# Kernel optimization log

Measured on AMD Instinct MI355X. Metric: run time of the kernel, lower is better.

The kernel has to match this reference:

```python
import jax, jax.numpy as jnp
import numpy as np

D_MODEL = 768; D_STATE = 64; D_CONV = 7; EXPAND = 2; HEADDIM = 64; NGROUPS = 1; CHUNK = 256
D_INNER = EXPAND * D_MODEL                                      # 1536
NHEADS = D_INNER // HEADDIM                                     # 24
D_IN_PROJ = 2 * D_INNER + 2 * NGROUPS * D_STATE + 2 * NHEADS    # 3248
CONV_DIM = D_INNER + 2 * NGROUPS * D_STATE                      # 1664
BATCH, SEQLEN = 2, 4096
EPS = 1e-5


def setup_inputs() -> dict:
    key = jax.random.key(0)
    ks = jax.random.split(key, 8)
    w = lambda k, shape, s=0.02: jax.random.normal(k, shape, jnp.float32) * s
    # dt in [1e-3, 1e-1], dt_bias = softplus^{-1}(dt)
    dt0 = jnp.exp(jax.random.uniform(ks[3], (NHEADS,)) * (np.log(0.1) - np.log(0.001)) + np.log(0.001))
    return {
        "x": jax.random.normal(ks[0], (BATCH, SEQLEN, D_MODEL), jnp.float32),
        "ln_w": jnp.ones((D_MODEL,), jnp.float32),
        "ln_b": jnp.zeros((D_MODEL,), jnp.float32),
        "in_proj_w": w(ks[1], (D_IN_PROJ, D_MODEL)),
        "conv_w": w(ks[2], (CONV_DIM, D_CONV), 0.2),
        "conv_b": jnp.zeros((CONV_DIM,), jnp.float32),
        "dt_bias": dt0 + jnp.log(-jnp.expm1(-dt0)),
        "A_log": jnp.log(jax.random.uniform(ks[4], (NHEADS,), minval=1.0, maxval=16.0)),
        "D": jnp.ones((NHEADS,), jnp.float32),
        "fc_D_w": w(ks[5], (NHEADS, D_INNER)),
        "rms_w": jnp.ones((D_INNER,), jnp.float32),
        "out_proj_w": w(ks[6], (D_MODEL, D_INNER)),
    }


def _segsum(a):
    # a: (..., T) -> (..., T, T) lower-triangular segment sums, -inf above diagonal
    T = a.shape[-1]
    cs = jnp.cumsum(a, -1)
    ss = cs[..., :, None] - cs[..., None, :]
    return jnp.where(jnp.tril(jnp.ones((T, T), bool)), ss, -jnp.inf)


def _ssd(X, A, Bm, Cm):
    # Chunked SSD scan (mamba_chunk_scan_combined, D=None, z=None, ngroups=1).
    # X: (b,l,h,p) already scaled by dt; A: (b,l,h) = dt*A_head; Bm,Cm: (b,l,n)
    b, l, h, p = X.shape
    c = l // CHUNK
    X = X.reshape(b, c, CHUNK, h, p)
    A = A.reshape(b, c, CHUNK, h).transpose(0, 3, 1, 2)  # (b,h,c,l)
    Bm = Bm.reshape(b, c, CHUNK, D_STATE)
    Cm = Cm.reshape(b, c, CHUNK, D_STATE)
    A_cum = jnp.cumsum(A, -1)
    Lmat = jnp.exp(_segsum(A))                                      # (b,h,c,l,s)
    Y_diag = jnp.einsum("bcln,bcsn,bhcls,bcshp->bclhp", Cm, Bm, Lmat, X)
    decay_states = jnp.exp(A_cum[..., -1:] - A_cum)                 # (b,h,c,l)
    states = jnp.einsum("bcln,bhcl,bclhp->bchpn", Bm, decay_states, X)
    A_chunk = jnp.pad(A_cum[..., -1], ((0, 0), (0, 0), (1, 0)))     # (b,h,c+1)
    decay_chunk = jnp.exp(_segsum(A_chunk))                         # (b,h,c+1,c+1)
    all_states = jnp.concatenate([jnp.zeros_like(states[:, :1]), states], 1)
    prev = jnp.einsum("bhzc,bchpn->bzhpn", decay_chunk, all_states)[:, :-1]
    Y_off = jnp.einsum("bcln,bchpn,bhcl->bclhp", Cm, prev, jnp.exp(A_cum))
    return (Y_diag + Y_off).reshape(b, l, h, p)


def _dwconv_causal(x, w, b):
    # x: (B,L,C), w: (C,K); torch Conv1d(padding=K-1) then [:, :L] == causal conv
    xp = jnp.pad(x, ((0, 0), (D_CONV - 1, 0), (0, 0))).transpose(0, 2, 1)
    y = jax.lax.conv_general_dilated(xp, w[:, None, :], (1,), "VALID",
                                     feature_group_count=CONV_DIM,
                                     dimension_numbers=("NCH", "OIH", "NCH"))
    return y.transpose(0, 2, 1) + b


def _forward(x, ln_w, ln_b, in_proj_w, conv_w, conv_b, dt_bias, A_log, D, fc_D_w, rms_w, out_proj_w):
    B, L, _ = x.shape
    # pre-LayerNorm
    mu = jnp.mean(x, -1, keepdims=True)
    var = jnp.mean((x - mu) ** 2, -1, keepdims=True)
    u = (x - mu) * jax.lax.rsqrt(var + EPS) * ln_w + ln_b
    # input projection -> z | xBC | dt_fw,dt_bw
    zxbcdt = u @ in_proj_w.T
    z = zxbcdt[..., :D_INNER]
    xBC = zxbcdt[..., D_INNER:D_INNER + CONV_DIM]
    dt2 = zxbcdt[..., -2 * NHEADS:]
    dt = jnp.concatenate([dt2[..., :NHEADS], jnp.flip(dt2[..., NHEADS:], 1)], 0)  # (2B,L,H)
    dt = jax.nn.softplus(dt + dt_bias)
    A = -jnp.exp(A_log)
    # causal depthwise conv + SiLU
    xBC = jax.nn.silu(_dwconv_causal(xBC, conv_w, conv_b))
    xs = xBC[..., :D_INNER]
    Bm = xBC[..., D_INNER:D_INNER + D_STATE]
    Cm = xBC[..., D_INNER + D_STATE:]
    x_og = xs
    cat2 = lambda t: jnp.concatenate([t, jnp.flip(t, 1)], 0)  # fwd + reversed copy
    X = cat2(xs).reshape(2 * B, L, NHEADS, HEADDIM) * dt[..., None]
    y = _ssd(X, dt * A, cat2(Bm), cat2(Cm)).reshape(2 * B, L, D_INNER)
    # quasiseparable combine: shift each direction by one, zero the boundary
    y = jnp.roll(y, 1, axis=1).at[:, 0, :].set(0.0)
    y = y[:B] + jnp.flip(y[B:], 1)
    # data-dependent diagonal term
    Dterm = x_og @ fc_D_w.T + D                                 # (B,L,H)
    y = y + x_og * jnp.repeat(Dterm, HEADDIM, axis=-1)
    # gated RMSNorm
    y = y * jax.nn.silu(z)
    y = y * jax.lax.rsqrt(jnp.mean(y * y, -1, keepdims=True) + EPS) * rms_w
    # out projection + residual (dropout=0 -> identity)
    return y @ out_proj_w.T + x


def reference(x, ln_w, ln_b, in_proj_w, conv_w, conv_b, dt_bias, A_log, D, fc_D_w, rms_w, out_proj_w):
    return _forward(x, ln_w, ln_b, in_proj_w, conv_w, conv_b, dt_bias, A_log, D, fc_D_w, rms_w, out_proj_w)
```

## Files before the change

kernel.cpp:

```cpp
#include <hip/hip_runtime.h>
#include <hip/hip_bf16.h>
#include <cstdint>
#include <cstddef>

typedef __hip_bfloat16 bf16;
typedef __attribute__((ext_vector_type(8))) short short8;
typedef __attribute__((ext_vector_type(4))) float f32x4;

#define B_   2
#define L_   4096
#define DM_  768
#define DI_  1536
#define NH_  24
#define HD_  64
#define DS_  64
#define CH_  256
#define NC_  16
#define CD_  1664
#define DIP_ 3248
#define EPS_ 1e-5f

#define ROWS_ (B_*L_)
#define BB4_  (2*B_)

#define LDSK 40
#define LDT  72

__device__ __forceinline__ float b2f(bf16 v) { return __bfloat162float(v); }
__device__ __forceinline__ bf16  f2b(float v) { return __float2bfloat16(v); }
__device__ __forceinline__ float sb2f(short s) {
    bf16 t; __builtin_memcpy(&t, &s, 2); return __bfloat162float(t);
}
__device__ __forceinline__ short f2s(float v) {
    bf16 t = __float2bfloat16(v); short s; __builtin_memcpy(&s, &t, 2); return s;
}

__global__ __launch_bounds__(256) void cast_f2b(const float* __restrict__ s,
                                                bf16* __restrict__ d, int n) {
    int i = (blockIdx.x * 256 + threadIdx.x) * 4;
    if (i + 3 < n) {
        float4 v = *(const float4*)(s + i);
        d[i]   = f2b(v.x); d[i+1] = f2b(v.y);
        d[i+2] = f2b(v.z); d[i+3] = f2b(v.w);
    } else {
        for (int k = i; k < n; k++) d[k] = f2b(s[k]);
    }
}

__global__ __launch_bounds__(256) void ln_kernel(const float* __restrict__ x,
                                                 const float* __restrict__ w,
                                                 const float* __restrict__ bb,
                                                 bf16* __restrict__ u) {
    int row = blockIdx.x, tid = threadIdx.x;
    const float* xr = x + (size_t)row * DM_;
    float v0 = xr[tid], v1 = xr[tid + 256], v2 = xr[tid + 512];
    float s = v0 + v1 + v2;
    float q = v0*v0 + v1*v1 + v2*v2;
    for (int off = 32; off > 0; off >>= 1) {
        s += __shfl_down(s, off);
        q += __shfl_down(q, off);
    }
    __shared__ float rs[4], rq[4];
    __shared__ float mean_s, rstd_s;
    int lane = tid & 63, wid = tid >> 6;
    if (!lane) { rs[wid] = s; rq[wid] = q; }
    __syncthreads();
    if (!tid) {
        float S = rs[0]+rs[1]+rs[2]+rs[3];
        float Q = rq[0]+rq[1]+rq[2]+rq[3];
        float mu = S / (float)DM_;
        float var = Q / (float)DM_ - mu*mu;
        mean_s = mu; rstd_s = rsqrtf(var + EPS_);
    }
    __syncthreads();
    float mu = mean_s, rstd = rstd_s;
    bf16* ur = u + (size_t)row * DM_;
    ur[tid]       = f2b((v0 - mu) * rstd * w[tid]       + bb[tid]);
    ur[tid + 256] = f2b((v1 - mu) * rstd * w[tid + 256] + bb[tid + 256]);
    ur[tid + 512] = f2b((v2 - mu) * rstd * w[tid + 512] + bb[tid + 512]);
}

__global__ __launch_bounds__(256) void gemm_bf16_inproj(const bf16* __restrict__ A,
                                                        const bf16* __restrict__ W,
                                                        bf16* __restrict__ zbuf,
                                                        bf16* __restrict__ xbc,
                                                        float* __restrict__ dtr) {
    __shared__ short As[128 * LDSK];
    __shared__ short Ws[128 * LDSK];
    int tid = threadIdx.x;
    int wave = tid >> 6, lane = tid & 63;
    int wm = (wave >> 1) * 64, wn = (wave & 1) * 64;
    int bm = blockIdx.y * 128, bn = blockIdx.x * 128;
    f32x4 acc[4][4] = {};
    int lr = tid >> 1;
    int lseg = (tid & 1) * 16;
    const int K = DM_;
    int fr = lane & 15, kg = (lane >> 4) * 8;
    for (int k0 = 0; k0 < K; k0 += 32) {
        const short* ag = (const short*)A + (size_t)(bm + lr) * K + k0 + lseg;
        short8 av0 = *(const short8*)ag;
        short8 av1 = *(const short8*)(ag + 8);
        short8 wv0 = {}, wv1 = {};
        int n = bn + lr;
        if (n < DIP_) {
            const short* wg = (const short*)W + (size_t)n * K + k0 + lseg;
            wv0 = *(const short8*)wg;
            wv1 = *(const short8*)(wg + 8);
        }
        __syncthreads();
        *(short8*)&As[lr*LDSK + lseg]     = av0;
        *(short8*)&As[lr*LDSK + lseg + 8] = av1;
        *(short8*)&Ws[lr*LDSK + lseg]     = wv0;
        *(short8*)&Ws[lr*LDSK + lseg + 8] = wv1;
        __syncthreads();
        short8 af[4], wf[4];
        #pragma unroll
        for (int i = 0; i < 4; i++)
            af[i] = *(const short8*)&As[(wm + i*16 + fr)*LDSK + kg];
        #pragma unroll
        for (int j = 0; j < 4; j++)
            wf[j] = *(const short8*)&Ws[(wn + j*16 + fr)*LDSK + kg];
        #pragma unroll
        for (int i = 0; i < 4; i++)
            #pragma unroll
            for (int j = 0; j < 4; j++)
                acc[i][j] = __builtin_amdgcn_mfma_f32_16x16x32_bf16(af[i], wf[j], acc[i][j], 0, 0, 0);
    }
    int rg = (lane >> 4) * 4;
    #pragma unroll
    for (int i = 0; i < 4; i++) {
        int mrow = bm + wm + i*16 + rg;
        #pragma unroll
        for (int j = 0; j < 4; j++) {
            int ncol = bn + wn + j*16 + fr;
            #pragma unroll
            for (int r = 0; r < 4; r++) {
                float v = acc[i][j][r];
                int m = mrow + r;
                if (ncol < DI_)            zbuf[(size_t)m * DI_ + ncol] = f2b(v);
                else if (ncol < DI_ + CD_) xbc[(size_t)m * CD_ + (ncol - DI_)] = f2b(v);
                else if (ncol < DIP_)      dtr[(size_t)m * 48 + (ncol - DI_ - CD_)] = v;
            }
        }
    }
}

__global__ __launch_bounds__(256) void gemm_bf16_out(const bf16* __restrict__ A,
                                                     const bf16* __restrict__ W,
                                                     const float* __restrict__ resid,
                                                     float* __restrict__ C) {
    __shared__ short As[128 * LDSK];
    __shared__ short Ws[128 * LDSK];
    int tid = threadIdx.x;
    int wave = tid >> 6, lane = tid & 63;
    int wm = (wave >> 1) * 64, wn = (wave & 1) * 64;
    int bm = blockIdx.y * 128, bn = blockIdx.x * 128;
    f32x4 acc[4][4] = {};
    int lr = tid >> 1;
    int lseg = (tid & 1) * 16;
    const int K = DI_;
    int fr = lane & 15, kg = (lane >> 4) * 8;
    for (int k0 = 0; k0 < K; k0 += 32) {
        const short* ag = (const short*)A + (size_t)(bm + lr) * K + k0 + lseg;
        short8 av0 = *(const short8*)ag;
        short8 av1 = *(const short8*)(ag + 8);
        const short* wg = (const short*)W + (size_t)(bn + lr) * K + k0 + lseg;
        short8 wv0 = *(const short8*)wg;
        short8 wv1 = *(const short8*)(wg + 8);
        __syncthreads();
        *(short8*)&As[lr*LDSK + lseg]     = av0;
        *(short8*)&As[lr*LDSK + lseg + 8] = av1;
        *(short8*)&Ws[lr*LDSK + lseg]     = wv0;
        *(short8*)&Ws[lr*LDSK + lseg + 8] = wv1;
        __syncthreads();
        short8 af[4], wf[4];
        #pragma unroll
        for (int i = 0; i < 4; i++)
            af[i] = *(const short8*)&As[(wm + i*16 + fr)*LDSK + kg];
        #pragma unroll
        for (int j = 0; j < 4; j++)
            wf[j] = *(const short8*)&Ws[(wn + j*16 + fr)*LDSK + kg];
        #pragma unroll
        for (int i = 0; i < 4; i++)
            #pragma unroll
            for (int j = 0; j < 4; j++)
                acc[i][j] = __builtin_amdgcn_mfma_f32_16x16x32_bf16(af[i], wf[j], acc[i][j], 0, 0, 0);
    }
    int rg = (lane >> 4) * 4;
    #pragma unroll
    for (int i = 0; i < 4; i++) {
        int mrow = bm + wm + i*16 + rg;
        #pragma unroll
        for (int j = 0; j < 4; j++) {
            int ncol = bn + wn + j*16 + fr;
            #pragma unroll
            for (int r = 0; r < 4; r++) {
                int m = mrow + r;
                C[(size_t)m * DM_ + ncol] = acc[i][j][r] + resid[(size_t)m * DM_ + ncol];
            }
        }
    }
}

__global__ __launch_bounds__(256) void conv_kernel(const bf16* __restrict__ xbc,
                                                   const float* __restrict__ cw,
                                                   const float* __restrict__ cb,
                                                   bf16* __restrict__ out) {
    int g = blockIdx.x * 256 + threadIdx.x;
    int cg = g % 208;
    int tq = g / 208;
    int b = tq >> 10;
    int t0 = (tq & 1023) * 4;
    int c8 = cg * 8;
    const short* src = (const short*)xbc + (size_t)(b * L_) * CD_ + c8;

    float w[7][8], acc[4][8];
    #pragma unroll
    for (int k = 0; k < 8; k++) {
        #pragma unroll
        for (int j = 0; j < 7; j++) w[j][k] = cw[(c8 + k) * 7 + j];
        float bias = cb[c8 + k];
        #pragma unroll
        for (int q = 0; q < 4; q++) acc[q][k] = bias;
    }
    #pragma unroll
    for (int m = 0; m < 10; m++) {
        int tt = t0 - 6 + m;
        float row[8];
        if (tt >= 0) {
            short8 v = *(const short8*)(src + (size_t)tt * CD_);
            #pragma unroll
            for (int k = 0; k < 8; k++) row[k] = sb2f(v[k]);
        } else {
            #pragma unroll
            for (int k = 0; k < 8; k++) row[k] = 0.f;
        }
        #pragma unroll
        for (int q = 0; q < 4; q++) {
            int j = m - q;
            if (j >= 0 && j < 7) {
                #pragma unroll
                for (int k = 0; k < 8; k++) acc[q][k] += row[k] * w[j][k];
            }
        }
    }
    #pragma unroll
    for (int q = 0; q < 4; q++) {
        short8 o;
        #pragma unroll
        for (int k = 0; k < 8; k++) {
            float a = acc[q][k];
            a = a / (1.f + __expf(-a));
            o[k] = f2s(a);
        }
        *(short8*)((short*)out + (size_t)(b * L_ + t0 + q) * CD_ + c8) = o;
    }
}

__global__ __launch_bounds__(256) void dt_kernel(const float* __restrict__ dtr,
                                                 const float* __restrict__ dt_bias,
                                                 float* __restrict__ dt4) {
    int idx = blockIdx.x * 256 + threadIdx.x;
    if (idx >= BB4_ * L_ * NH_) return;
    int h = idx % NH_;
    int t = (idx / NH_) % L_;
    int bbx = idx / (NH_ * L_);
    int bp = bbx & 1;
    float raw;
    if (bbx < 2) raw = dtr[((size_t)(bp * L_ + t)) * 48 + h];
    else         raw = dtr[((size_t)(bp * L_ + (L_ - 1 - t))) * 48 + NH_ + h];
    float v = raw + dt_bias[h];
    float dt = (v > 20.f) ? v : log1pf(__expf(v));
    dt4[idx] = dt;
}

__global__ __launch_bounds__(256) void scan_kernel(const float* __restrict__ dt4,
                                                   const float* __restrict__ A_log,
                                                   float* __restrict__ Acum) {
    int bid = blockIdx.x;
    int c  = bid % NC_;
    int h  = (bid / NC_) % NH_;
    int bbx = bid / (NC_ * NH_);
    int l = threadIdx.x;
    float Ah = -__expf(A_log[h]);
    float val = dt4[((size_t)(bbx * L_) + c * CH_ + l) * NH_ + h] * Ah;
    __shared__ float sc[256];
    sc[l] = val; __syncthreads();
    for (int off = 1; off < 256; off <<= 1) {
        float t = (l >= off) ? sc[l - off] : 0.f;
        __syncthreads();
        sc[l] += t;
        __syncthreads();
    }
    Acum[(size_t)bid * CH_ + l] = sc[l];
}

__global__ __launch_bounds__(256) void xt_kernel(const bf16* __restrict__ conv,
                                                 const float* __restrict__ dt4,
                                                 bf16* __restrict__ XT,
                                                 bf16* __restrict__ BT) {
    int bid = blockIdx.x;
    int hh = bid % 25;
    int c  = (bid / 25) % NC_;
    int bbx = bid / (25 * NC_);
    int bp = bbx & 1;
    bool flip = bbx >= 2;
    bool isB = (hh == NH_);
    int coff = isB ? DI_ : hh * HD_;
    int tid = threadIdx.x;
    __shared__ short tile[64][72];
    short* dstb = (short*)(isB ? BT : XT);
    size_t rowbase = isB ? (size_t)(bbx * 64) : (size_t)((bbx * NH_ + hh) * 64);
    for (int lt = 0; lt < 4; lt++) {
        __syncthreads();
        #pragma unroll
        for (int it = 0; it < 2; it++) {
            int li = tid + it * 256;
            int r = li >> 3, seg = (li & 7) * 8;
            int t = c * CH_ + lt * 64 + r;
            int tt = flip ? (L_ - 1 - t) : t;
            short8 v = *(const short8*)((const short*)conv + (size_t)(bp * L_ + tt) * CD_ + coff + seg);
            if (!isB) {
                float dtv = dt4[((size_t)(bbx * L_) + t) * NH_ + hh];
                #pragma unroll
                for (int k = 0; k < 8; k++) v[k] = f2s(sb2f(v[k]) * dtv);
            }
            *(short8*)&tile[r][seg] = v;
        }
        __syncthreads();
        #pragma unroll
        for (int it = 0; it < 2; it++) {
            int li = tid + it * 256;
            int p = li >> 3, seg = (li & 7) * 8;
            short8 o;
            #pragma unroll
            for (int k = 0; k < 8; k++) o[k] = tile[seg + k][p];
            *(short8*)(dstb + (rowbase + p) * L_ + c * CH_ + lt * 64 + seg) = o;
        }
    }
}

__global__ __launch_bounds__(256) void states_kernel(const bf16* __restrict__ XT,
                                                     const bf16* __restrict__ BT,
                                                     const float* __restrict__ Acum,
                                                     bf16* __restrict__ states) {
    int bid = blockIdx.x;
    int h = bid % NH_;
    int c = (bid / NH_) % NC_;
    int bbx = bid / (NH_ * NC_);
    int tid = threadIdx.x;
    int wave = tid >> 6, lane = tid & 63;
    int wr = wave >> 1, wc = wave & 1;
    int fr = lane & 15, kg = (lane >> 4) * 8, rg = (lane >> 4) * 4;
    size_t abase = ((size_t)(bbx * NH_ + h) * NC_ + c) * CH_;
    __shared__ float dec[256];
    {
        float Atot = Acum[abase + CH_ - 1];
        dec[tid] = __expf(Atot - Acum[abase + tid]);
    }
    __syncthreads();
    const short* xbase = (const short*)XT + (size_t)((bbx * NH_ + h) * 64) * L_ + c * CH_;
    const short* bbase = (const short*)BT + (size_t)(bbx * 64) * L_ + c * CH_;
    f32x4 acc[2][2] = {};
    for (int lt = 0; lt < 4; lt++) {
        #pragma unroll
        for (int ks = 0; ks < 2; ks++) {
            int l0 = lt * 64 + ks * 32 + kg;
            float d[8];
            #pragma unroll
            for (int k = 0; k < 8; k++) d[k] = dec[l0 + k];
            short8 af[2], wf[2];
            #pragma unroll
            for (int i = 0; i < 2; i++)
                af[i] = *(const short8*)(xbase + (size_t)(wr*32 + i*16 + fr) * L_ + l0);
            #pragma unroll
            for (int j = 0; j < 2; j++) {
                short8 raw = *(const short8*)(bbase + (size_t)(wc*32 + j*16 + fr) * L_ + l0);
                #pragma unroll
                for (int k = 0; k < 8; k++) raw[k] = f2s(sb2f(raw[k]) * d[k]);
                wf[j] = raw;
            }
            #pragma unroll
            for (int i = 0; i < 2; i++)
                #pragma unroll
                for (int j = 0; j < 2; j++)
                    acc[i][j] = __builtin_amdgcn_mfma_f32_16x16x32_bf16(af[i], wf[j], acc[i][j], 0, 0, 0);
        }
    }
    size_t sbase = (size_t)bid * 4096;
    #pragma unroll
    for (int i = 0; i < 2; i++)
        #pragma unroll
        for (int j = 0; j < 2; j++)
            #pragma unroll
            for (int r = 0; r < 4; r++) {
                int p = wr*32 + i*16 + rg + r;
                int n = wc*32 + j*16 + fr;
                states[sbase + p*64 + n] = f2b(acc[i][j][r]);
            }
}

__global__ __launch_bounds__(256) void chunkscan_kernel(bf16* __restrict__ sp,
                                                        const float* __restrict__ Acum) {
    int bid = blockIdx.x;
    int h = bid % NH_;
    int bbx = bid / NH_;
    int tid = threadIdx.x;
    float run[16];
    #pragma unroll
    for (int k = 0; k < 16; k++) run[k] = 0.f;
    for (int c = 0; c < NC_; c++) {
        float Tc = Acum[((size_t)(bbx * NH_ + h) * NC_ + c) * CH_ + CH_ - 1];
        float ec = __expf(Tc);
        size_t base = ((size_t)(bbx * NC_ + c) * NH_ + h) * 4096;
        #pragma unroll
        for (int k = 0; k < 16; k++) {
            size_t e = tid + k * 256;
            float sv = b2f(sp[base + e]);
            sp[base + e] = f2b(run[k]);
            run[k] = run[k] * ec + sv;
        }
    }
}

__global__ __launch_bounds__(256) void ydiag_kernel(const bf16* __restrict__ conv,
                                                    const bf16* __restrict__ XT,
                                                    const float* __restrict__ Acum,
                                                    const bf16* __restrict__ prev,
                                                    bf16* __restrict__ yc,
                                                    int pass) {
    int bid = blockIdx.x;
    int lt = bid & 3;
    int q  = bid >> 2;
    int h  = q % NH_;
    int r2 = q / NH_;
    int c  = r2 % NC_;
    int b  = r2 / NC_;
    int bbx = pass ? (b + 2) : b;
    int bp = b;
    bool flip = pass != 0;
    int tid = threadIdx.x;
    int wave = tid >> 6, lane = tid & 63;
    int wr = wave >> 1, wc = wave & 1;
    int fr = lane & 15, kg = (lane >> 4) * 8, rg = (lane >> 4) * 4;
    size_t abase = ((size_t)(bbx * NH_ + h) * NC_ + c) * CH_;

    __shared__ short Gt[64 * LDT];
    __shared__ float aL[64], aS[64];
    if (tid < 64) aL[tid] = Acum[abase + lt * 64 + tid];

    short8 cf[2][2];
    #pragma unroll
    for (int i = 0; i < 2; i++) {
        int l = wr*32 + i*16 + fr;
        int t = c * CH_ + lt * 64 + l;
        int tt = flip ? (L_ - 1 - t) : t;
        const short* crow = (const short*)conv + (size_t)(bp * L_ + tt) * CD_ + DI_ + DS_;
        #pragma unroll
        for (int ks = 0; ks < 2; ks++)
            cf[i][ks] = *(const short8*)(crow + ks*32 + kg);
    }

    f32x4 acc[2][2] = {};
    size_t pbase = ((size_t)(bbx * NC_ + c) * NH_ + h) * 4096;
    #pragma unroll
    for (int ks = 0; ks < 2; ks++) {
        #pragma unroll
        for (int j = 0; j < 2; j++) {
            short8 pf = *(const short8*)((const short*)prev + pbase + (size_t)(wc*32 + j*16 + fr)*64 + ks*32 + kg);
            #pragma unroll
            for (int i = 0; i < 2; i++)
                acc[i][j] = __builtin_amdgcn_mfma_f32_16x16x32_bf16(cf[i][ks], pf, acc[i][j], 0, 0, 0);
        }
    }
    __syncthreads();
    #pragma unroll
    for (int i = 0; i < 2; i++)
        #pragma unroll
        for (int r = 0; r < 4; r++) {
            float e = __expf(aL[wr*32 + i*16 + rg + r]);
            #pragma unroll
            for (int j = 0; j < 2; j++) acc[i][j][r] *= e;
        }

    const short* xbase = (const short*)XT + (size_t)((bbx * NH_ + h) * 64) * L_ + c * CH_;

    for (int st = 0; st <= lt; st++) {
        if (tid < 64) aS[tid] = Acum[abase + st * 64 + tid];
        f32x4 gacc[2][2] = {};
        #pragma unroll
        for (int j = 0; j < 2; j++) {
            int s = wc*32 + j*16 + fr;
            int t = c * CH_ + st * 64 + s;
            int tt = flip ? (L_ - 1 - t) : t;
            const short* brow = (const short*)conv + (size_t)(bp * L_ + tt) * CD_ + DI_;
            #pragma unroll
            for (int ks = 0; ks < 2; ks++) {
                short8 bf = *(const short8*)(brow + ks*32 + kg);
                #pragma unroll
                for (int i = 0; i < 2; i++)
                    gacc[i][j] = __builtin_amdgcn_mfma_f32_16x16x32_bf16(cf[i][ks], bf, gacc[i][j], 0, 0, 0);
            }
        }
        __syncthreads();
        #pragma unroll
        for (int i = 0; i < 2; i++)
            #pragma unroll
            for (int j = 0; j < 2; j++)
                #pragma unroll
                for (int r = 0; r < 4; r++) {
                    int ll = wr*32 + i*16 + rg + r;
                    int ss = wc*32 + j*16 + fr;
                    bool valid = (st < lt) || (ll >= ss);
                    float g = valid ? gacc[i][j][r] * __expf(aL[ll] - aS[ss]) : 0.f;
                    Gt[ll * LDT + ss] = f2s(g);
                }
        __syncthreads();
        #pragma unroll
        for (int ks = 0; ks < 2; ks++) {
            short8 gf[2], xf[2];
            #pragma unroll
            for (int i = 0; i < 2; i++)
                gf[i] = *(const short8*)&Gt[(wr*32 + i*16 + fr)*LDT + ks*32 + kg];
            #pragma unroll
            for (int j = 0; j < 2; j++)
                xf[j] = *(const short8*)(xbase + (size_t)(wc*32 + j*16 + fr)*L_ + st*64 + ks*32 + kg);
            #pragma unroll
            for (int i = 0; i < 2; i++)
                #pragma unroll
                for (int j = 0; j < 2; j++)
                    acc[i][j] = __builtin_amdgcn_mfma_f32_16x16x32_bf16(gf[i], xf[j], acc[i][j], 0, 0, 0);
        }
        __syncthreads();
    }

    #pragma unroll
    for (int i = 0; i < 2; i++)
        #pragma unroll
        for (int r = 0; r < 4; r++) {
            int l = wr*32 + i*16 + rg + r;
            int t = c * CH_ + lt * 64 + l;
            #pragma unroll
            for (int j = 0; j < 2; j++) {
                int p = wc*32 + j*16 + fr;
                float v = acc[i][j][r];
                if (!pass) {
                    int pos = t + 1;
                    if (pos == L_)
                        yc[((size_t)(b * L_)) * DI_ + h * HD_ + p] = f2b(0.f);
                    else
                        yc[((size_t)(b * L_) + pos) * DI_ + h * HD_ + p] = f2b(v);
                } else {
                    int pos = L_ - 2 - t;
                    if (pos >= 0) {
                        size_t o = ((size_t)(b * L_) + pos) * DI_ + h * HD_ + p;
                        yc[o] = f2b(b2f(yc[o]) + v);
                    }
                }
            }
        }
}

__global__ __launch_bounds__(256) void combine_kernel(const bf16* __restrict__ yc,
                                                      const bf16* __restrict__ conv,
                                                      const bf16* __restrict__ zbuf,
                                                      const float* __restrict__ fcD,
                                                      const float* __restrict__ Dvec,
                                                      const float* __restrict__ rms_w,
                                                      bf16* __restrict__ ybuf) {
    int row = blockIdx.x;
    int tid = threadIdx.x;
    __shared__ float xog_s[DI_];
    __shared__ float dterm_s[NH_];
    __shared__ float rs[4];
    __shared__ float scale_s;
    float yv[6], xog[6], zv[6];
    const bf16* convrow = conv + (size_t)row * CD_;
    const bf16* zrow = zbuf + (size_t)row * DI_;
    const bf16* ycrow = yc + (size_t)row * DI_;
    #pragma unroll
    for (int k = 0; k < 6; k++) {
        int d = tid + k * 256;
        float xo = b2f(convrow[d]);
        xog[k] = xo; xog_s[d] = xo;
        zv[k] = b2f(zrow[d]);
        yv[k] = b2f(ycrow[d]);
    }
    __syncthreads();
    int wid = tid >> 6, lane = tid & 63;
    for (int hh = 0; hh < 6; hh++) {
        int h = wid * 6 + hh;
        float s = 0.f;
        #pragma unroll
        for (int k = 0; k < 24; k++) {
            int d = lane + k * 64;
            s += xog_s[d] * fcD[(size_t)h * DI_ + d];
        }
        for (int off = 32; off > 0; off >>= 1) s += __shfl_down(s, off);
        if (!lane) dterm_s[h] = s + Dvec[h];
    }
    __syncthreads();
    float ss = 0.f;
    #pragma unroll
    for (int k = 0; k < 6; k++) {
        int d = tid + k * 256;
        int h = d >> 6;
        float y = yv[k] + xog[k] * dterm_s[h];
        float z = zv[k];
        y *= z / (1.f + __expf(-z));
        yv[k] = y;
        ss += y * y;
    }
    for (int off = 32; off > 0; off >>= 1) ss += __shfl_down(ss, off);
    if (!lane) rs[wid] = ss;
    __syncthreads();
    if (!tid) scale_s = rsqrtf((rs[0]+rs[1]+rs[2]+rs[3]) / (float)DI_ + EPS_);
    __syncthreads();
    float sc = scale_s;
    bf16* yrow = ybuf + (size_t)row * DI_;
    #pragma unroll
    for (int k = 0; k < 6; k++) {
        int d = tid + k * 256;
        yrow[d] = f2b(yv[k] * sc * rms_w[d]);
    }
}

extern "C" void kernel_launch(void* const* d_in, const int* in_sizes, int n_in,
                              void* d_out, int out_size, void* d_ws, size_t ws_size,
                              hipStream_t stream) {
    const float* x        = (const float*)d_in[0];
    const float* ln_w     = (const float*)d_in[1];
    const float* ln_b     = (const float*)d_in[2];
    const float* in_proj  = (const float*)d_in[3];
    const float* conv_w   = (const float*)d_in[4];
    const float* conv_b   = (const float*)d_in[5];
    const float* dt_bias  = (const float*)d_in[6];
    const float* A_log    = (const float*)d_in[7];
    const float* Dvec     = (const float*)d_in[8];
    const float* fc_D_w   = (const float*)d_in[9];
    const float* rms_w    = (const float*)d_in[10];
    const float* out_proj = (const float*)d_in[11];
    float* out = (float*)d_out;

    uint8_t* base = (uint8_t*)d_ws;
    size_t off = 0;
    auto alloc = [&](size_t bytes) -> void* {
        void* p = base + off;
        off += (bytes + 255) & ~(size_t)255;
        return p;
    };
    bf16*  buf_z    = (bf16*) alloc((size_t)ROWS_ * DI_ * 2);
    uint8_t* regA   = (uint8_t*)alloc((size_t)ROWS_ * CD_ * 2);
    float* buf_dtr  = (float*)alloc((size_t)ROWS_ * 48 * 4);
    bf16*  buf_conv = (bf16*) alloc((size_t)ROWS_ * CD_ * 2);
    float* buf_dt   = (float*)alloc((size_t)BB4_ * L_ * NH_ * 4);
    float* buf_acum = (float*)alloc((size_t)BB4_ * NH_ * NC_ * CH_ * 4);
    uint8_t* regB   = (uint8_t*)alloc((size_t)ROWS_ * DM_ * 4);
    bf16*  w_in_bf  = (bf16*) alloc((size_t)DIP_ * DM_ * 2);
    bf16*  w_out_bf = (bf16*) alloc((size_t)DM_ * DI_ * 2);
    bf16*  buf_XT   = (bf16*) alloc((size_t)BB4_ * NH_ * 64 * L_ * 2);
    bf16*  buf_BT   = (bf16*) alloc((size_t)BB4_ * 64 * L_ * 2);

    bf16*  buf_xbc  = (bf16*)regA;
    bf16*  buf_sp   = (bf16*)regA;
    bf16*  buf_y    = (bf16*)regA;
    bf16*  buf_u    = (bf16*)regB;
    bf16*  buf_yc   = (bf16*)regB;

    cast_f2b<<<(DIP_ * DM_ / 4 + 255) / 256, 256, 0, stream>>>(in_proj, w_in_bf, DIP_ * DM_);
    cast_f2b<<<(DM_ * DI_ / 4 + 255) / 256, 256, 0, stream>>>(out_proj, w_out_bf, DM_ * DI_);
    ln_kernel<<<ROWS_, 256, 0, stream>>>(x, ln_w, ln_b, buf_u);
    gemm_bf16_inproj<<<dim3((DIP_ + 127) / 128, ROWS_ / 128), 256, 0, stream>>>(
        buf_u, w_in_bf, buf_z, buf_xbc, buf_dtr);
    conv_kernel<<<(ROWS_ / 4) * (CD_ / 8) / 256, 256, 0, stream>>>(buf_xbc, conv_w, conv_b, buf_conv);
    dt_kernel<<<(BB4_ * L_ * NH_) / 256, 256, 0, stream>>>(buf_dtr, dt_bias, buf_dt);
    scan_kernel<<<BB4_ * NH_ * NC_, 256, 0, stream>>>(buf_dt, A_log, buf_acum);
    xt_kernel<<<BB4_ * NC_ * 25, 256, 0, stream>>>(buf_conv, buf_dt, buf_XT, buf_BT);
    states_kernel<<<BB4_ * NC_ * NH_, 256, 0, stream>>>(buf_XT, buf_BT, buf_acum, buf_sp);
    chunkscan_kernel<<<BB4_ * NH_, 256, 0, stream>>>(buf_sp, buf_acum);
    ydiag_kernel<<<B_ * NC_ * NH_ * 4, 256, 0, stream>>>(buf_conv, buf_XT, buf_acum, buf_sp, buf_yc, 0);
    ydiag_kernel<<<B_ * NC_ * NH_ * 4, 256, 0, stream>>>(buf_conv, buf_XT, buf_acum, buf_sp, buf_yc, 1);
    combine_kernel<<<ROWS_, 256, 0, stream>>>(buf_yc, buf_conv, buf_z, fc_D_w, Dvec, rms_w, buf_y);
    gemm_bf16_out<<<dim3(DM_ / 128, ROWS_ / 128), 256, 0, stream>>>(
        buf_y, w_out_bf, x, out);
}
```

Baseline: 532.6 us.

## Use direct global-to-LDS loads in GEMMs and merge ydiag passes

Both GEMMs now stage A and W tiles with global_load_lds 16-byte transfers into an XOR-swizzled unpadded LDS layout, skipping the register round trip. The in_proj weight is padded to 3328 rows so the bounds check goes away. The two ydiag launches become one launch that writes the forward and backward outputs to separate buffers, which removes the read-modify-write accumulation. The shift-and-add combine moves into combine_kernel, at the cost of an extra activation buffer and an extra read per row.

Result: slower. 545.0 us (+2.3%).

```diff
diff --git a/kernel.cpp b/kernel.cpp
--- a/kernel.cpp
+++ b/kernel.cpp
@@ -18,12 +18,12 @@
 #define NC_  16
 #define CD_  1664
 #define DIP_ 3248
+#define NPAD_ 3328
 #define EPS_ 1e-5f
 
 #define ROWS_ (B_*L_)
 #define BB4_  (2*B_)
 
-#define LDSK 40
 #define LDT  72
 
 __device__ __forceinline__ float b2f(bf16 v) { return __bfloat162float(v); }
@@ -33,6 +33,11 @@
 }
 __device__ __forceinline__ short f2s(float v) {
     bf16 t = __float2bfloat16(v); short s; __builtin_memcpy(&s, &t, 2); return s;
+}
+__device__ __forceinline__ void gl_lds16(const void* g, void* l) {
+    __builtin_amdgcn_global_load_lds((const __attribute__((address_space(1))) unsigned int*)g,
+                                     (__attribute__((address_space(3))) unsigned int*)l,
+                                     16, 0, 0);
 }
 
 __global__ __launch_bounds__(256) void cast_f2b(const float* __restrict__ s,
@@ -44,6 +49,22 @@
         d[i+2] = f2b(v.z); d[i+3] = f2b(v.w);
     } else {
         for (int k = i; k < n; k++) d[k] = f2b(s[k]);
+    }
+}
+
+__global__ __launch_bounds__(256) void cast_pad_inproj(const float* __restrict__ s,
+                                                       bf16* __restrict__ d) {
+    int i = (blockIdx.x * 256 + threadIdx.x) * 4;
+    const int nsrc = DIP_ * DM_;
+    const int ntot = NPAD_ * DM_;
+    if (i >= ntot) return;
+    if (i + 3 < nsrc) {
+        float4 v = *(const float4*)(s + i);
+        d[i]   = f2b(v.x); d[i+1] = f2b(v.y);
+        d[i+2] = f2b(v.z); d[i+3] = f2b(v.w);
+    } else {
+        for (int k = i; k < i + 4 && k < ntot; k++)
+            d[k] = (k < nsrc) ? f2b(s[k]) : f2b(0.f);
     }
 }
 
@@ -80,46 +101,42 @@
     ur[tid + 512] = f2b((v2 - mu) * rstd * w[tid + 512] + bb[tid + 512]);
 }
 
-__global__ __launch_bounds__(256) void gemm_bf16_inproj(const bf16* __restrict__ A,
-                                                        const bf16* __restrict__ W,
-                                                        bf16* __restrict__ zbuf,
-                                                        bf16* __restrict__ xbc,
-                                                        float* __restrict__ dtr) {
-    __shared__ short As[128 * LDSK];
-    __shared__ short Ws[128 * LDSK];
+__global__ __launch_bounds__(256) void gemm_gl_inproj(const bf16* __restrict__ A,
+                                                      const bf16* __restrict__ W,
+                                                      bf16* __restrict__ zbuf,
+                                                      bf16* __restrict__ xbc,
+                                                      float* __restrict__ dtr) {
+    __shared__ short As[128 * 32];
+    __shared__ short Ws[128 * 32];
     int tid = threadIdx.x;
     int wave = tid >> 6, lane = tid & 63;
     int wm = (wave >> 1) * 64, wn = (wave & 1) * 64;
     int bm = blockIdx.y * 128, bn = blockIdx.x * 128;
+    int fr = lane & 15, g = lane >> 4;
+    const int K = DM_;
+    int srow = lane >> 2;
+    int scol = ((lane & 3) ^ ((lane >> 3) & 3)) * 8;
+    int rsl = (g ^ ((fr >> 1) & 3)) * 8;
+    const short* Ag = (const short*)A;
+    const short* Wg = (const short*)W;
     f32x4 acc[4][4] = {};
-    int lr = tid >> 1;
-    int lseg = (tid & 1) * 16;
-    const int K = DM_;
-    int fr = lane & 15, kg = (lane >> 4) * 8;
     for (int k0 = 0; k0 < K; k0 += 32) {
-        const short* ag = (const short*)A + (size_t)(bm + lr) * K + k0 + lseg;
-        short8 av0 = *(const short8*)ag;
-        short8 av1 = *(const short8*)(ag + 8);
-        short8 wv0 = {}, wv1 = {};
-        int n = bn + lr;
-        if (n < DIP_) {
-            const short* wg = (const short*)W + (size_t)n * K + k0 + lseg;
-            wv0 = *(const short8*)wg;
-            wv1 = *(const short8*)(wg + 8);
-        }
-        __syncthreads();
-        *(short8*)&As[lr*LDSK + lseg]     = av0;
-        *(short8*)&As[lr*LDSK + lseg + 8] = av1;
-        *(short8*)&Ws[lr*LDSK + lseg]     = wv0;
-        *(short8*)&Ws[lr*LDSK + lseg + 8] = wv1;
+        __syncthreads();
+        #pragma unroll
+        for (int q = 0; q < 2; q++) {
+            gl_lds16(Ag + (size_t)(bm + q*64 + wave*16 + srow) * K + k0 + scol,
+                     &As[(q*64 + wave*16) * 32]);
+            gl_lds16(Wg + (size_t)(bn + q*64 + wave*16 + srow) * K + k0 + scol,
+                     &Ws[(q*64 + wave*16) * 32]);
+        }
         __syncthreads();
         short8 af[4], wf[4];
         #pragma unroll
         for (int i = 0; i < 4; i++)
-            af[i] = *(const short8*)&As[(wm + i*16 + fr)*LDSK + kg];
+            af[i] = *(const short8*)&As[(wm + i*16 + fr)*32 + rsl];
         #pragma unroll
         for (int j = 0; j < 4; j++)
-            wf[j] = *(const short8*)&Ws[(wn + j*16 + fr)*LDSK + kg];
+            wf[j] = *(const short8*)&Ws[(wn + j*16 + fr)*32 + rsl];
         #pragma unroll
         for (int i = 0; i < 4; i++)
             #pragma unroll
@@ -145,41 +162,41 @@
     }
 }
 
-__global__ __launch_bounds__(256) void gemm_bf16_out(const bf16* __restrict__ A,
-                                                     const bf16* __restrict__ W,
-                                                     const float* __restrict__ resid,
-                                                     float* __restrict__ C) {
-    __shared__ short As[128 * LDSK];
-    __shared__ short Ws[128 * LDSK];
+__global__ __launch_bounds__(256) void gemm_gl_out(const bf16* __restrict__ A,
+                                                   const bf16* __restrict__ W,
+                                                   const float* __restrict__ resid,
+                                                   float* __restrict__ C) {
+    __shared__ short As[128 * 32];
+    __shared__ short Ws[128 * 32];
     int tid = threadIdx.x;
     int wave = tid >> 6, lane = tid & 63;
     int wm = (wave >> 1) * 64, wn = (wave & 1) * 64;
     int bm = blockIdx.y * 128, bn = blockIdx.x * 128;
+    int fr = lane & 15, g = lane >> 4;
+    const int K = DI_;
+    int srow = lane >> 2;
+    int scol = ((lane & 3) ^ ((lane >> 3) & 3)) * 8;
+    int rsl = (g ^ ((fr >> 1) & 3)) * 8;
+    const short* Ag = (const short*)A;
+    const short* Wg = (const short*)W;
     f32x4 acc[4][4] = {};
-    int lr = tid >> 1;
-    int lseg = (tid & 1) * 16;
-    const int K = DI_;
-    int fr = lane & 15, kg = (lane >> 4) * 8;
     for (int k0 = 0; k0 < K; k0 += 32) {
-        const short* ag = (const short*)A + (size_t)(bm + lr) * K + k0 + lseg;
-        short8 av0 = *(const short8*)ag;
-        short8 av1 = *(const short8*)(ag + 8);
-        const short* wg = (const short*)W + (size_t)(bn + lr) * K + k0 + lseg;
-        short8 wv0 = *(const short8*)wg;
-        short8 wv1 = *(const short8*)(wg + 8);
-        __syncthreads();
-        *(short8*)&As[lr*LDSK + lseg]     = av0;
-        *(short8*)&As[lr*LDSK + lseg + 8] = av1;
-        *(short8*)&Ws[lr*LDSK + lseg]     = wv0;
-        *(short8*)&Ws[lr*LDSK + lseg + 8] = wv1;
+        __syncthreads();
+        #pragma unroll
+        for (int q = 0; q < 2; q++) {
+            gl_lds16(Ag + (size_t)(bm + q*64 + wave*16 + srow) * K + k0 + scol,
+                     &As[(q*64 + wave*16) * 32]);
+            gl_lds16(Wg + (size_t)(bn + q*64 + wave*16 + srow) * K + k0 + scol,
+                     &Ws[(q*64 + wave*16) * 32]);
+        }
         __syncthreads();
         short8 af[4], wf[4];
         #pragma unroll
         for (int i = 0; i < 4; i++)
-            af[i] = *(const short8*)&As[(wm + i*16 + fr)*LDSK + kg];
+            af[i] = *(const short8*)&As[(wm + i*16 + fr)*32 + rsl];
         #pragma unroll
         for (int j = 0; j < 4; j++)
-            wf[j] = *(const short8*)&Ws[(wn + j*16 + fr)*LDSK + kg];
+            wf[j] = *(const short8*)&Ws[(wn + j*16 + fr)*32 + rsl];
         #pragma unroll
         for (int i = 0; i < 4; i++)
             #pragma unroll
@@ -427,18 +444,17 @@
                                                     const bf16* __restrict__ XT,
                                                     const float* __restrict__ Acum,
                                                     const bf16* __restrict__ prev,
-                                                    bf16* __restrict__ yc,
-                                                    int pass) {
+                                                    bf16* __restrict__ yf,
+                                                    bf16* __restrict__ yb) {
     int bid = blockIdx.x;
     int lt = bid & 3;
     int q  = bid >> 2;
     int h  = q % NH_;
     int r2 = q / NH_;
     int c  = r2 % NC_;
-    int b  = r2 / NC_;
-    int bbx = pass ? (b + 2) : b;
-    int bp = b;
-    bool flip = pass != 0;
+    int bbx = r2 / NC_;
+    int bp = bbx & 1;
+    bool flip = bbx >= 2;
     int tid = threadIdx.x;
     int wave = tid >> 6, lane = tid & 63;
     int wr = wave >> 1, wc = wave & 1;
@@ -496,10 +512,10 @@
             const short* brow = (const short*)conv + (size_t)(bp * L_ + tt) * CD_ + DI_;
             #pragma unroll
             for (int ks = 0; ks < 2; ks++) {
-                short8 bf = *(const short8*)(brow + ks*32 + kg);
+                short8 bfv = *(const short8*)(brow + ks*32 + kg);
                 #pragma unroll
                 for (int i = 0; i < 2; i++)
-                    gacc[i][j] = __builtin_amdgcn_mfma_f32_16x16x32_bf16(cf[i][ks], bf, gacc[i][j], 0, 0, 0);
+                    gacc[i][j] = __builtin_amdgcn_mfma_f32_16x16x32_bf16(cf[i][ks], bfv, gacc[i][j], 0, 0, 0);
             }
         }
         __syncthreads();
@@ -512,8 +528,8 @@
                     int ll = wr*32 + i*16 + rg + r;
                     int ss = wc*32 + j*16 + fr;
                     bool valid = (st < lt) || (ll >= ss);
-                    float g = valid ? gacc[i][j][r] * __expf(aL[ll] - aS[ss]) : 0.f;
-                    Gt[ll * LDT + ss] = f2s(g);
+                    float gv = valid ? gacc[i][j][r] * __expf(aL[ll] - aS[ss]) : 0.f;
+                    Gt[ll * LDT + ss] = f2s(gv);
                 }
         __syncthreads();
         #pragma unroll
@@ -534,6 +550,7 @@
         __syncthreads();
     }
 
+    bf16* dst = flip ? yb : yf;
     #pragma unroll
     for (int i = 0; i < 2; i++)
         #pragma unroll
@@ -543,25 +560,13 @@
             #pragma unroll
             for (int j = 0; j < 2; j++) {
                 int p = wc*32 + j*16 + fr;
-                float v = acc[i][j][r];
-                if (!pass) {
-                    int pos = t + 1;
-                    if (pos == L_)
-                        yc[((size_t)(b * L_)) * DI_ + h * HD_ + p] = f2b(0.f);
-                    else
-                        yc[((size_t)(b * L_) + pos) * DI_ + h * HD_ + p] = f2b(v);
-                } else {
-                    int pos = L_ - 2 - t;
-                    if (pos >= 0) {
-                        size_t o = ((size_t)(b * L_) + pos) * DI_ + h * HD_ + p;
-                        yc[o] = f2b(b2f(yc[o]) + v);
-                    }
-                }
-            }
-        }
-}
-
-__global__ __launch_bounds__(256) void combine_kernel(const bf16* __restrict__ yc,
+                dst[((size_t)(bp * L_) + t) * DI_ + h * HD_ + p] = f2b(acc[i][j][r]);
+            }
+        }
+}
+
+__global__ __launch_bounds__(256) void combine_kernel(const bf16* __restrict__ yf,
+                                                      const bf16* __restrict__ yb,
                                                       const bf16* __restrict__ conv,
                                                       const bf16* __restrict__ zbuf,
                                                       const float* __restrict__ fcD,
@@ -569,6 +574,8 @@
                                                       const float* __restrict__ rms_w,
                                                       bf16* __restrict__ ybuf) {
     int row = blockIdx.x;
+    int b = row >> 12;
+    int t = row & (L_ - 1);
     int tid = threadIdx.x;
     __shared__ float xog_s[DI_];
     __shared__ float dterm_s[NH_];
@@ -577,14 +584,17 @@
     float yv[6], xog[6], zv[6];
     const bf16* convrow = conv + (size_t)row * CD_;
     const bf16* zrow = zbuf + (size_t)row * DI_;
-    const bf16* ycrow = yc + (size_t)row * DI_;
+    const bf16* yfr = (t > 0) ? (yf + (size_t)(row - 1) * DI_) : nullptr;
+    const bf16* ybr = (t < L_ - 1) ? (yb + ((size_t)(b * L_) + (L_ - 2 - t)) * DI_) : nullptr;
     #pragma unroll
     for (int k = 0; k < 6; k++) {
         int d = tid + k * 256;
         float xo = b2f(convrow[d]);
         xog[k] = xo; xog_s[d] = xo;
         zv[k] = b2f(zrow[d]);
-        yv[k] = b2f(ycrow[d]);
+        float y1 = yfr ? b2f(yfr[d]) : 0.f;
+        float y2 = ybr ? b2f(ybr[d]) : 0.f;
+        yv[k] = y1 + y2;
     }
     __syncthreads();
     int wid = tid >> 6, lane = tid & 63;
@@ -656,7 +666,8 @@
     float* buf_dt   = (float*)alloc((size_t)BB4_ * L_ * NH_ * 4);
     float* buf_acum = (float*)alloc((size_t)BB4_ * NH_ * NC_ * CH_ * 4);
     uint8_t* regB   = (uint8_t*)alloc((size_t)ROWS_ * DM_ * 4);
-    bf16*  w_in_bf  = (bf16*) alloc((size_t)DIP_ * DM_ * 2);
+    bf16*  buf_yb   = (bf16*) alloc((size_t)B_ * L_ * DI_ * 2);
+    bf16*  w_in_bf  = (bf16*) alloc((size_t)NPAD_ * DM_ * 2);
     bf16*  w_out_bf = (bf16*) alloc((size_t)DM_ * DI_ * 2);
     bf16*  buf_XT   = (bf16*) alloc((size_t)BB4_ * NH_ * 64 * L_ * 2);
     bf16*  buf_BT   = (bf16*) alloc((size_t)BB4_ * 64 * L_ * 2);
@@ -665,12 +676,12 @@
     bf16*  buf_sp   = (bf16*)regA;
     bf16*  buf_y    = (bf16*)regA;
     bf16*  buf_u    = (bf16*)regB;
-    bf16*  buf_yc   = (bf16*)regB;
-
-    cast_f2b<<<(DIP_ * DM_ / 4 + 255) / 256, 256, 0, stream>>>(in_proj, w_in_bf, DIP_ * DM_);
+    bf16*  buf_yf   = (bf16*)regB;
+
+    cast_pad_inproj<<<(NPAD_ * DM_ / 4 + 255) / 256, 256, 0, stream>>>(in_proj, w_in_bf);
     cast_f2b<<<(DM_ * DI_ / 4 + 255) / 256, 256, 0, stream>>>(out_proj, w_out_bf, DM_ * DI_);
     ln_kernel<<<ROWS_, 256, 0, stream>>>(x, ln_w, ln_b, buf_u);
-    gemm_bf16_inproj<<<dim3((DIP_ + 127) / 128, ROWS_ / 128), 256, 0, stream>>>(
+    gemm_gl_inproj<<<dim3(NPAD_ / 128, ROWS_ / 128), 256, 0, stream>>>(
         buf_u, w_in_bf, buf_z, buf_xbc, buf_dtr);
     conv_kernel<<<(ROWS_ / 4) * (CD_ / 8) / 256, 256, 0, stream>>>(buf_xbc, conv_w, conv_b, buf_conv);
     dt_kernel<<<(BB4_ * L_ * NH_) / 256, 256, 0, stream>>>(buf_dtr, dt_bias, buf_dt);
@@ -678,9 +689,8 @@
     xt_kernel<<<BB4_ * NC_ * 25, 256, 0, stream>>>(buf_conv, buf_dt, buf_XT, buf_BT);
     states_kernel<<<BB4_ * NC_ * NH_, 256, 0, stream>>>(buf_XT, buf_BT, buf_acum, buf_sp);
     chunkscan_kernel<<<BB4_ * NH_, 256, 0, stream>>>(buf_sp, buf_acum);
-    ydiag_kernel<<<B_ * NC_ * NH_ * 4, 256, 0, stream>>>(buf_conv, buf_XT, buf_acum, buf_sp, buf_yc, 0);
-    ydiag_kernel<<<B_ * NC_ * NH_ * 4, 256, 0, stream>>>(buf_conv, buf_XT, buf_acum, buf_sp, buf_yc, 1);
-    combine_kernel<<<ROWS_, 256, 0, stream>>>(buf_yc, buf_conv, buf_z, fc_D_w, Dvec, rms_w, buf_y);
-    gemm_bf16_out<<<dim3(DM_ / 128, ROWS_ / 128), 256, 0, stream>>>(
+    ydiag_kernel<<<BB4_ * NC_ * NH_ * 4, 256, 0, stream>>>(buf_conv, buf_XT, buf_acum, buf_sp, buf_yf, buf_yb);
+    combine_kernel<<<ROWS_, 256, 0, stream>>>(buf_yf, buf_yb, buf_conv, buf_z, fc_D_w, Dvec, rms_w, buf_y);
+    gemm_gl_out<<<dim3(DM_ / 128, ROWS_ / 128), 256, 0, stream>>>(
         buf_y, w_out_bf, x, out);
 }
```
